# Kernel optimization log

Measured on AMD Instinct MI355X. Metric: run time of the kernel, lower is better.

The kernel has to match this reference:

```python
import jax, jax.numpy as jnp
import numpy as np

N, SEQ_LEN, HORIZON, F_IN, EMBED, HIDDEN, LAYERS = 4096, 168, 24, 32, 32, 64, 2
G4 = 4 * HIDDEN
# NOTE: original torch code calls nn.LSTM per-step WITHOUT carrying hidden state,
# so each step's LSTM starts from (h0=0, c0=0): W_hh contributes nothing, only b_hh.

def setup_inputs() -> dict:
    key = jax.random.key(0)
    ks = jax.random.split(key, 12)
    s = 0.1
    return {
        "X": jax.random.normal(ks[0], (N, SEQ_LEN, F_IN), jnp.float32),
        "y": jax.random.normal(ks[1], (N, SEQ_LEN), jnp.float32),
        "Xf": jax.random.normal(ks[2], (N, HORIZON, F_IN), jnp.float32),
        "W_embed": jax.random.normal(ks[3], (EMBED, 1), jnp.float32) * s,
        "b_embed": jax.random.normal(ks[4], (EMBED,), jnp.float32) * s,
        "W_ih": jax.random.normal(ks[5], (LAYERS, G4, EMBED + F_IN), jnp.float32) * s,  # layer1 in-dim == HIDDEN == EMBED+F_IN
        "b_ih": jax.random.normal(ks[6], (LAYERS, G4), jnp.float32) * s,
        "b_hh": jax.random.normal(ks[7], (LAYERS, G4), jnp.float32) * s,
        "W_mu": jax.random.normal(ks[8], (1, HIDDEN), jnp.float32) * s,
        "b_mu": jax.random.normal(ks[9], (1,), jnp.float32) * s,
        "W_sigma": jax.random.normal(ks[10], (1, HIDDEN), jnp.float32) * s,
        "b_sigma": jax.random.normal(ks[11], (1,), jnp.float32) * s,
    }


def reference(X, y, Xf, W_embed, b_embed, W_ih, b_ih, b_hh, W_mu, b_mu, W_sigma, b_sigma):
    num_ts = X.shape[0]
    T = SEQ_LEN + HORIZON
    Xall = jnp.concatenate([X, Xf], axis=1)  # (N, T, F_IN)
    y_pad = jnp.concatenate([y, jnp.zeros((num_ts, HORIZON), y.dtype)], axis=1)  # (N, T)
    use_y = jnp.arange(T) < SEQ_LEN  # teacher-forced region

    def step(carry, inputs):
        x_s, y_s, use = inputs  # (N, F_IN), (N,), scalar bool
        ynext = jnp.where(use, y_s[:, None], carry)  # (N, 1)
        yembed = ynext @ W_embed.T + b_embed  # (N, EMBED)
        h = jnp.concatenate([x_s, yembed], axis=1)  # (N, F_IN+EMBED)
        for l in range(LAYERS):  # single LSTM step from zero state per layer
            gates = h @ W_ih[l].T + b_ih[l] + b_hh[l]  # (N, 4H); torch gate order i,f,g,o
            i_g, f_g, g_g, o_g = jnp.split(gates, 4, axis=1)
            c = jax.nn.sigmoid(i_g) * jnp.tanh(g_g)  # f * c0 term vanishes (c0 = 0)
            h = jax.nn.sigmoid(o_g) * jnp.tanh(c)
        h = jax.nn.relu(h)
        mu = h @ W_mu.T + b_mu  # (N, 1)
        sigma = jax.nn.softplus(h @ W_sigma.T + b_sigma) + 1e-6  # log(1+exp(.)) + eps
        lik = (2.0 * np.pi * sigma ** 2) ** (-0.5) * jnp.exp(-((ynext - mu) ** 2) / (2.0 * sigma ** 2))
        return lik, (lik[:, 0], mu[:, 0], sigma[:, 0])

    carry0 = jnp.zeros((num_ts, 1), X.dtype)
    xs = (jnp.swapaxes(Xall, 0, 1), y_pad.T, use_y)
    _, (lik_t, mu_t, sigma_t) = jax.lax.scan(step, carry0, xs)  # each (T, N)
    ypred = lik_t.T[:, SEQ_LEN - 1: SEQ_LEN + HORIZON - 1]  # (N, HORIZON)
    return ypred, mu_t.T, sigma_t.T
```

## Files before the change

kernel.cpp:

```cpp
#include <hip/hip_runtime.h>
#include <math.h>

#define N_TS 4096
#define SEQ  168
#define HOR  24
#define T_ALL 192
#define F_INP 32
#define HID  64
#define NROW 192
#define NB_B (N_TS / 16)
#define L2E  1.44269504089f

typedef _Float16 half8  __attribute__((ext_vector_type(8)));
typedef _Float16 half4  __attribute__((ext_vector_type(4)));
typedef float    floatx4 __attribute__((ext_vector_type(4)));

__device__ __forceinline__ float fexp(float x)  { return __expf(x); }
__device__ __forceinline__ float ex2(float x)   { return __builtin_amdgcn_exp2f(x); }
__device__ __forceinline__ float frcp(float x)  { return __builtin_amdgcn_rcpf(x); }
__device__ __forceinline__ float softplus_(float x) { return (x > 15.0f) ? x : __logf(1.0f + fexp(x)); }

__device__ __forceinline__ float lstm_h(float ip, float gp, float op) {
    const float Ei = ex2(ip);
    const float Eg = ex2(gp);
    const float cc = (1.0f - Eg) * frcp((1.0f + Ei) * (1.0f + Eg));
    const float Ec = ex2(cc * (-2.0f * L2E));
    const float Eo = ex2(op);
    return (1.0f - Ec) * frcp((1.0f + Ec) * (1.0f + Eo));
}

__device__ __forceinline__ half8 cvt8(const float4 a, const float4 b) {
    half8 v;
    v[0]=(_Float16)a.x; v[1]=(_Float16)a.y; v[2]=(_Float16)a.z; v[3]=(_Float16)a.w;
    v[4]=(_Float16)b.x; v[5]=(_Float16)b.y; v[6]=(_Float16)b.z; v[7]=(_Float16)b.w;
    return v;
}

__global__ __launch_bounds__(256) void prep(
    const float* __restrict__ W_ih, const float* __restrict__ b_ih,
    const float* __restrict__ b_hh,
    const float* __restrict__ W_embed, const float* __restrict__ b_embed,
    _Float16* __restrict__ W16f, float* __restrict__ bsum,
    float* __restrict__ wy1, float* __restrict__ b1c)
{
    const int idx = blockIdx.x * 256 + threadIdx.x;
    for (int i = idx; i < 2 * 8 * NROW * 8; i += gridDim.x * 256) {
        const int kp  = i & 7;
        const int row = (i >> 3) % NROW;
        const int kb  = ((i >> 3) / NROW) & 7;
        const int l   = i / (8 * NROW * 8);
        const int sr  = (row < 64) ? row : row + 64;
        const float sc = (row >= 64 && row < 128) ? (-2.0f * L2E) : (-L2E);
        W16f[i] = (_Float16)(W_ih[(l * 256 + sr) * HID + kb * 8 + kp] * sc);
    }
    for (int i = idx; i < 2 * NROW; i += gridDim.x * 256) {
        const int r = i % NROW;
        const int l = i / NROW;
        const int sr = (r < 64) ? r : r + 64;
        const float sc = (r >= 64 && r < 128) ? (-2.0f * L2E) : (-L2E);
        bsum[i] = (b_ih[l * 256 + sr] + b_hh[l * 256 + sr]) * sc;
    }
    if (idx < NROW) {
        const int sr = (idx < 64) ? idx : idx + 64;
        const float sc = (idx >= 64 && idx < 128) ? (-2.0f * L2E) : (-L2E);
        const float* wrow = W_ih + sr * HID + 32;
        float s1 = 0.f, s2 = 0.f;
        #pragma unroll
        for (int k = 0; k < 32; ++k) {
            s1 = fmaf(wrow[k], W_embed[k], s1);
            s2 = fmaf(wrow[k], b_embed[k], s2);
        }
        wy1[idx] = s1 * sc;
        b1c[idx] = (b_ih[sr] + b_hh[sr] + s2) * sc;
    }
}

__global__ __launch_bounds__(256, 5) void fused(
    const float* __restrict__ X,
    const float* __restrict__ y,
    const float* __restrict__ Xf,
    const float* __restrict__ W_embed,
    const float* __restrict__ b_embed,
    const _Float16* __restrict__ W16f,
    const float* __restrict__ bsum,
    const float* __restrict__ wy1,
    const float* __restrict__ b1c,
    const float* __restrict__ W_mu,
    const float* __restrict__ b_mu,
    const float* __restrict__ W_sigma,
    const float* __restrict__ b_sigma,
    float* __restrict__ out)
{
    __shared__ union __align__(16) {
        struct { _Float16 Wl[12288]; _Float16 Hx[4][1024]; } A;
        struct { _Float16 slab[16 * 64]; float partm[16][4]; float parts[16][4];
                 float wyb[NROW]; float b1cb[NROW]; } B;
    } sh;

    const int tid = threadIdx.x;
    float* mu_out = out + (size_t)N_TS * HOR;
    float* sg_out = mu_out + (size_t)N_TS * T_ALL;

    if (blockIdx.x < NB_B) {
        __builtin_amdgcn_s_setprio(1);
        const int w    = tid >> 6;
        const int lane = tid & 63;
        const int quad = lane >> 4;
        const int ln   = lane & 15;
        const int n0   = blockIdx.x * 16;

        if (tid < NROW) {
            sh.B.wyb[tid]  = wy1[tid];
            sh.B.b1cb[tid] = b1c[tid];
        }

        half8 B1[3];
        half8 B2[3][2];
        float bias2[3];
        #pragma unroll
        for (int j = 0; j < 3; ++j) {
            const int rt = j * 4 + w;
            B1[j] = *(const half8*)(W16f + ((size_t)quad * NROW + rt * 16 + ln) * 8);
            #pragma unroll
            for (int kt = 0; kt < 2; ++kt)
                B2[j][kt] = *(const half8*)(W16f + 12288 + ((size_t)(kt * 4 + quad) * NROW + rt * 16 + ln) * 8);
            bias2[j] = bsum[NROW + rt * 16 + ln];
        }
        const float wmu = W_mu[w * 16 + ln], wsg = W_sigma[w * 16 + ln];
        const float bmu = b_mu[0], bsg = b_sigma[0];

        const float* xfp = Xf + (size_t)(n0 + ln) * HOR * F_INP + quad * 8;
        float4 xa, xb;
        {
            const float* xp = X + ((size_t)(n0 + ln) * SEQ + (SEQ - 1)) * F_INP + quad * 8;
            xa = *(const float4*)xp;
            xb = *(const float4*)(xp + 4);
        }
        float ycur = y[(size_t)(n0 + ln) * SEQ + (SEQ - 1)];
        __syncthreads();

        #pragma unroll 1
        for (int it = 0; it <= HOR + 1; ++it) {
            if (it > 0) {
                const int k = it - 1;
                const float4 m4 = *(const float4*)sh.B.partm[ln];
                const float4 s4 = *(const float4*)sh.B.parts[ln];
                const float mu = (m4.x + m4.y) + (m4.z + m4.w) + bmu;
                const float sg = softplus_((s4.x + s4.y) + (s4.z + s4.w) + bsg) + 1e-6f;
                const float d  = ycur - mu;
                const float is = frcp(sg);
                const float lik = 0.39894228040143267f * is * fexp(-0.5f * d * d * is * is);
                if (k > 0 && w == 0 && quad == 0) {
                    const int nn = n0 + ln;
                    const int t  = SEQ + k - 1;
                    mu_out[(size_t)nn * T_ALL + t] = mu;
                    sg_out[(size_t)nn * T_ALL + t] = sg;
                    if (k < HOR) out[(size_t)nn * HOR + k] = lik;
                }
                ycur = lik;
            }
            if (it > HOR) break;

            const half8 xf0 = cvt8(xa, xb);
            if (it < HOR) {
                xa = *(const float4*)(xfp + it * F_INP);
                xb = *(const float4*)(xfp + it * F_INP + 4);
            }

            floatx4 t0 = *(const floatx4*)(sh.B.b1cb + 0 * 64 + w * 16 + quad * 4);
            floatx4 t1 = *(const floatx4*)(sh.B.b1cb + 1 * 64 + w * 16 + quad * 4);
            floatx4 t2 = *(const floatx4*)(sh.B.b1cb + 2 * 64 + w * 16 + quad * 4);
            t0 = __builtin_amdgcn_mfma_f32_16x16x32_f16(B1[0], xf0, t0, 0, 0, 0);
            t1 = __builtin_amdgcn_mfma_f32_16x16x32_f16(B1[1], xf0, t1, 0, 0, 0);
            t2 = __builtin_amdgcn_mfma_f32_16x16x32_f16(B1[2], xf0, t2, 0, 0, 0);

            const floatx4 wy0 = *(const floatx4*)(sh.B.wyb + 0 * 64 + w * 16 + quad * 4);
            const floatx4 wy1v = *(const floatx4*)(sh.B.wyb + 1 * 64 + w * 16 + quad * 4);
            const floatx4 wy2 = *(const floatx4*)(sh.B.wyb + 2 * 64 + w * 16 + quad * 4);

            half4 h1p;
            #pragma unroll
            for (int r = 0; r < 4; ++r) {
                const float ig = fmaf(ycur, wy0[r], t0[r]);
                const float gg = fmaf(ycur, wy1v[r], t1[r]);
                const float og = fmaf(ycur, wy2[r], t2[r]);
                h1p[r] = (_Float16)lstm_h(ig, gg, og);
            }
            {
                const int xblk = (2 * w + (quad >> 1)) ^ (ln & 7);
                *(half4*)(&sh.B.slab[ln * 64 + xblk * 8 + (quad & 1) * 4]) = h1p;
            }
            __syncthreads();

            const half8 a0 = *(const half8*)(&sh.B.slab[ln * 64 + ((quad ^ (ln & 7)) << 3)]);
            const half8 a1 = *(const half8*)(&sh.B.slab[ln * 64 + (((4 + quad) ^ (ln & 7)) << 3)]);
            floatx4 acc[3];
            #pragma unroll
            for (int j = 0; j < 3; ++j) {
                acc[j] = (floatx4){bias2[j], bias2[j], bias2[j], bias2[j]};
                acc[j] = __builtin_amdgcn_mfma_f32_16x16x32_f16(a0, B2[j][0], acc[j], 0, 0, 0);
                acc[j] = __builtin_amdgcn_mfma_f32_16x16x32_f16(a1, B2[j][1], acc[j], 0, 0, 0);
            }

            float pmr[4], psr[4];
            #pragma unroll
            for (int r = 0; r < 4; ++r) {
                const float hh = lstm_h(acc[0][r], acc[1][r], acc[2][r]);
                const float hr = fmaxf(hh, 0.0f);
                pmr[r] = hr * wmu;
                psr[r] = hr * wsg;
            }
            #pragma unroll
            for (int off = 1; off < 16; off <<= 1) {
                #pragma unroll
                for (int r = 0; r < 4; ++r) {
                    pmr[r] += __shfl_xor(pmr[r], off, 64);
                    psr[r] += __shfl_xor(psr[r], off, 64);
                }
            }
            if (ln == 0) {
                #pragma unroll
                for (int r = 0; r < 4; ++r) {
                    sh.B.partm[quad * 4 + r][w] = pmr[r];
                    sh.B.parts[quad * 4 + r][w] = psr[r];
                }
            }
            __syncthreads();
        }
        return;
    }

    const int w    = tid >> 6;
    const int lane = tid & 63;
    const int quad = lane >> 4;
    const int ln   = lane & 15;
    const int cid0 = (blockIdx.x - NB_B) * 64 + w * 16;
    const int cid  = cid0 + ln;

    half8 afr0, afr1;
    {
        const float* xp = X + (size_t)cid * F_INP + quad * 8;
        const float4 xa = *(const float4*)xp;
        const float4 xb = *(const float4*)(xp + 4);
        afr0 = cvt8(xa, xb);
        const float yv = y[cid];
        const float4 wa = *(const float4*)(W_embed + quad * 8);
        const float4 wb = *(const float4*)(W_embed + quad * 8 + 4);
        const float4 ba = *(const float4*)(b_embed + quad * 8);
        const float4 bb = *(const float4*)(b_embed + quad * 8 + 4);
        afr1[0]=(_Float16)fmaf(yv, wa.x, ba.x); afr1[1]=(_Float16)fmaf(yv, wa.y, ba.y);
        afr1[2]=(_Float16)fmaf(yv, wa.z, ba.z); afr1[3]=(_Float16)fmaf(yv, wa.w, ba.w);
        afr1[4]=(_Float16)fmaf(yv, wb.x, bb.x); afr1[5]=(_Float16)fmaf(yv, wb.y, bb.y);
        afr1[6]=(_Float16)fmaf(yv, wb.z, bb.z); afr1[7]=(_Float16)fmaf(yv, wb.w, bb.w);
    }

    #pragma unroll
    for (int c = 0; c < 6; ++c) {
        const int off = (c * 256 + tid) * 8;
        *(half8*)(sh.A.Wl + off) = *(const half8*)(W16f + off);
    }
    __syncthreads();

    _Float16* hrow = sh.A.Hx[w];
    {
        const _Float16* bp = sh.A.Wl + quad * 1536 + ln * 8;
        #pragma unroll
        for (int jt = 0; jt < 4; ++jt) {
            const float bi = bsum[jt * 16 + ln];
            const float bg = bsum[(4 + jt) * 16 + ln];
            const float bo = bsum[(8 + jt) * 16 + ln];
            floatx4 ai = (floatx4){bi, bi, bi, bi};
            floatx4 ag = (floatx4){bg, bg, bg, bg};
            floatx4 ao = (floatx4){bo, bo, bo, bo};
            ai = __builtin_amdgcn_mfma_f32_16x16x32_f16(afr0, *(const half8*)(bp + jt * 128),              ai, 0, 0, 0);
            ai = __builtin_amdgcn_mfma_f32_16x16x32_f16(afr1, *(const half8*)(bp + jt * 128 + 6144),       ai, 0, 0, 0);
            ag = __builtin_amdgcn_mfma_f32_16x16x32_f16(afr0, *(const half8*)(bp + (4 + jt) * 128),        ag, 0, 0, 0);
            ag = __builtin_amdgcn_mfma_f32_16x16x32_f16(afr1, *(const half8*)(bp + (4 + jt) * 128 + 6144), ag, 0, 0, 0);
            ao = __builtin_amdgcn_mfma_f32_16x16x32_f16(afr0, *(const half8*)(bp + (8 + jt) * 128),        ao, 0, 0, 0);
            ao = __builtin_amdgcn_mfma_f32_16x16x32_f16(afr1, *(const half8*)(bp + (8 + jt) * 128 + 6144), ao, 0, 0, 0);
            #pragma unroll
            for (int r = 0; r < 4; ++r) {
                const float hh = lstm_h(ai[r], ag[r], ao[r]);
                const int row = quad * 4 + r;
                const int col = jt * 16 + ln;
                hrow[row * 64 + (((col >> 3) ^ (row & 7)) << 3) + (col & 7)] = (_Float16)hh;
            }
        }
    }

    const half8 a0 = *(const half8*)(hrow + ln * 64 + ((quad ^ (ln & 7)) << 3));
    const half8 a1 = *(const half8*)(hrow + ln * 64 + (((4 + quad) ^ (ln & 7)) << 3));

    __syncthreads();
    #pragma unroll
    for (int c = 0; c < 6; ++c) {
        const int off = (c * 256 + tid) * 8;
        *(half8*)(sh.A.Wl + off) = *(const half8*)(W16f + 12288 + off);
    }
    __syncthreads();

    float hfin[4][4];
    {
        const _Float16* bp = sh.A.Wl + quad * 1536 + ln * 8;
        #pragma unroll
        for (int jt = 0; jt < 4; ++jt) {
            const float bi = bsum[NROW + jt * 16 + ln];
            const float bg = bsum[NROW + (4 + jt) * 16 + ln];
            const float bo = bsum[NROW + (8 + jt) * 16 + ln];
            floatx4 ai = (floatx4){bi, bi, bi, bi};
            floatx4 ag = (floatx4){bg, bg, bg, bg};
            floatx4 ao = (floatx4){bo, bo, bo, bo};
            ai = __builtin_amdgcn_mfma_f32_16x16x32_f16(a0, *(const half8*)(bp + jt * 128),              ai, 0, 0, 0);
            ai = __builtin_amdgcn_mfma_f32_16x16x32_f16(a1, *(const half8*)(bp + jt * 128 + 6144),       ai, 0, 0, 0);
            ag = __builtin_amdgcn_mfma_f32_16x16x32_f16(a0, *(const half8*)(bp + (4 + jt) * 128),        ag, 0, 0, 0);
            ag = __builtin_amdgcn_mfma_f32_16x16x32_f16(a1, *(const half8*)(bp + (4 + jt) * 128 + 6144), ag, 0, 0, 0);
            ao = __builtin_amdgcn_mfma_f32_16x16x32_f16(a0, *(const half8*)(bp + (8 + jt) * 128),        ao, 0, 0, 0);
            ao = __builtin_amdgcn_mfma_f32_16x16x32_f16(a1, *(const half8*)(bp + (8 + jt) * 128 + 6144), ao, 0, 0, 0);
            #pragma unroll
            for (int r = 0; r < 4; ++r)
                hfin[jt][r] = lstm_h(ai[r], ag[r], ao[r]);
        }
    }

    float wmu[4], wsg[4];
    #pragma unroll
    for (int jt = 0; jt < 4; ++jt) {
        wmu[jt] = W_mu[jt * 16 + ln];
        wsg[jt] = W_sigma[jt * 16 + ln];
    }
    const float bmu = b_mu[0], bsg = b_sigma[0];

    #pragma unroll
    for (int r = 0; r < 4; ++r) {
        float pm = 0.f, ps = 0.f;
        #pragma unroll
        for (int jt = 0; jt < 4; ++jt) {
            const float hr = fmaxf(hfin[jt][r], 0.0f);
            pm = fmaf(hr, wmu[jt], pm);
            ps = fmaf(hr, wsg[jt], ps);
        }
        #pragma unroll
        for (int off = 1; off < 16; off <<= 1) {
            pm += __shfl_xor(pm, off, 64);
            ps += __shfl_xor(ps, off, 64);
        }
        if (ln == 0) {
            const int cid2 = cid0 + quad * 4 + r;
            const int n = cid2 / SEQ;
            const int t = cid2 - n * SEQ;
            const float mu = pm + bmu;
            const float sg = softplus_(ps + bsg) + 1e-6f;
            mu_out[(size_t)n * T_ALL + t] = mu;
            sg_out[(size_t)n * T_ALL + t] = sg;
            if (t == SEQ - 1) {
                const float yv = y[cid2];
                const float d  = yv - mu;
                const float is = frcp(sg);
                const float lik = 0.39894228040143267f * is * fexp(-0.5f * d * d * is * is);
                out[(size_t)n * HOR] = lik;
            }
        }
    }
}

extern "C" void kernel_launch(void* const* d_in, const int* in_sizes, int n_in,
                              void* d_out, int out_size, void* d_ws, size_t ws_size,
                              hipStream_t stream) {
    const float* X       = (const float*)d_in[0];
    const float* y       = (const float*)d_in[1];
    const float* Xf      = (const float*)d_in[2];
    const float* W_embed = (const float*)d_in[3];
    const float* b_embed = (const float*)d_in[4];
    const float* W_ih    = (const float*)d_in[5];
    const float* b_ih    = (const float*)d_in[6];
    const float* b_hh    = (const float*)d_in[7];
    const float* W_mu    = (const float*)d_in[8];
    const float* b_mu    = (const float*)d_in[9];
    const float* W_sigma = (const float*)d_in[10];
    const float* b_sigma = (const float*)d_in[11];

    float* out = (float*)d_out;
    _Float16*  W16f = (_Float16*)d_ws;
    float*     bsum = (float*)((char*)d_ws + 49152);
    float*     wy1  = (float*)((char*)d_ws + 49152 + 1536);
    float*     b1c  = (float*)((char*)d_ws + 49152 + 1536 + 768);

    prep<<<96, 256, 0, stream>>>(W_ih, b_ih, b_hh, W_embed, b_embed,
                                 W16f, bsum, wy1, b1c);

    fused<<<NB_B + (N_TS * SEQ) / 64, 256, 0, stream>>>(
        X, y, Xf, W_embed, b_embed, W16f, bsum, wy1, b1c,
        W_mu, b_mu, W_sigma, b_sigma, out);
}
```

Before: 249.1 us.

## Fold y-embedding into layer-1 bias, halve layer-1 K, and use 512-thread blocks

The teacher-forced blocks now treat the y-embedding half of layer 1 as a rank-1 term (y*wy1 + b1c) instead of a second K=32 MFMA. This halves layer-1 MFMA work and shrinks the packed layer-1 weights. Blocks grow to 512 threads: autoregressive blocks handle two 16-series groups with separate shared-memory slabs, and teacher-forced blocks cover 128 rows. The mu/sigma head is restructured to use an operand-swapped MFMA layout with a shorter cross-lane reduction, and half-width stores of h. Larger blocks may cut occupancy flexibility and increase the cost of each barrier.

```diff
diff --git a/kernel.cpp b/kernel.cpp
--- a/kernel.cpp
+++ b/kernel.cpp
@@ -8,8 +8,10 @@
 #define F_INP 32
 #define HID  64
 #define NROW 192
-#define NB_B (N_TS / 16)
+#define NB_B (N_TS / 32)
+#define NT_B ((N_TS * SEQ) / 128)
 #define L2E  1.44269504089f
+#define W16F_L1 6144
 
 typedef _Float16 half8  __attribute__((ext_vector_type(8)));
 typedef _Float16 half4  __attribute__((ext_vector_type(4)));
@@ -44,14 +46,21 @@
     float* __restrict__ wy1, float* __restrict__ b1c)
 {
     const int idx = blockIdx.x * 256 + threadIdx.x;
-    for (int i = idx; i < 2 * 8 * NROW * 8; i += gridDim.x * 256) {
+    for (int i = idx; i < 4 * NROW * 8; i += gridDim.x * 256) {
         const int kp  = i & 7;
         const int row = (i >> 3) % NROW;
-        const int kb  = ((i >> 3) / NROW) & 7;
-        const int l   = i / (8 * NROW * 8);
+        const int kb  = (i >> 3) / NROW;
         const int sr  = (row < 64) ? row : row + 64;
         const float sc = (row >= 64 && row < 128) ? (-2.0f * L2E) : (-L2E);
-        W16f[i] = (_Float16)(W_ih[(l * 256 + sr) * HID + kb * 8 + kp] * sc);
+        W16f[i] = (_Float16)(W_ih[sr * HID + kb * 8 + kp] * sc);
+    }
+    for (int i = idx; i < 8 * NROW * 8; i += gridDim.x * 256) {
+        const int kp  = i & 7;
+        const int row = (i >> 3) % NROW;
+        const int kb  = (i >> 3) / NROW;
+        const int sr  = (row < 64) ? row : row + 64;
+        const float sc = (row >= 64 && row < 128) ? (-2.0f * L2E) : (-L2E);
+        W16f[W16F_L1 + i] = (_Float16)(W_ih[(256 + sr) * HID + kb * 8 + kp] * sc);
     }
     for (int i = idx; i < 2 * NROW; i += gridDim.x * 256) {
         const int r = i % NROW;
@@ -75,7 +84,7 @@
     }
 }
 
-__global__ __launch_bounds__(256, 5) void fused(
+__global__ __launch_bounds__(512, 8) void fused(
     const float* __restrict__ X,
     const float* __restrict__ y,
     const float* __restrict__ Xf,
@@ -92,8 +101,8 @@
     float* __restrict__ out)
 {
     __shared__ union __align__(16) {
-        struct { _Float16 Wl[12288]; _Float16 Hx[4][1024]; } A;
-        struct { _Float16 slab[16 * 64]; float partm[16][4]; float parts[16][4];
+        struct { _Float16 Wl[12288]; _Float16 Hx[8][1024]; } A;
+        struct { _Float16 slab[2][1024]; float partm[2][16][4]; float parts[2][16][4];
                  float wyb[NROW]; float b1cb[NROW]; } B;
     } sh;
 
@@ -104,10 +113,12 @@
     if (blockIdx.x < NB_B) {
         __builtin_amdgcn_s_setprio(1);
         const int w    = tid >> 6;
+        const int g    = w >> 2;
+        const int wg   = w & 3;
         const int lane = tid & 63;
         const int quad = lane >> 4;
         const int ln   = lane & 15;
-        const int n0   = blockIdx.x * 16;
+        const int n0   = blockIdx.x * 32 + g * 16;
 
         if (tid < NROW) {
             sh.B.wyb[tid]  = wy1[tid];
@@ -119,14 +130,14 @@
         float bias2[3];
         #pragma unroll
         for (int j = 0; j < 3; ++j) {
-            const int rt = j * 4 + w;
+            const int rt = j * 4 + wg;
             B1[j] = *(const half8*)(W16f + ((size_t)quad * NROW + rt * 16 + ln) * 8);
             #pragma unroll
             for (int kt = 0; kt < 2; ++kt)
-                B2[j][kt] = *(const half8*)(W16f + 12288 + ((size_t)(kt * 4 + quad) * NROW + rt * 16 + ln) * 8);
+                B2[j][kt] = *(const half8*)(W16f + W16F_L1 + ((size_t)(kt * 4 + quad) * NROW + rt * 16 + ln) * 8);
             bias2[j] = bsum[NROW + rt * 16 + ln];
         }
-        const float wmu = W_mu[w * 16 + ln], wsg = W_sigma[w * 16 + ln];
+        const float wmu = W_mu[wg * 16 + ln], wsg = W_sigma[wg * 16 + ln];
         const float bmu = b_mu[0], bsg = b_sigma[0];
 
         const float* xfp = Xf + (size_t)(n0 + ln) * HOR * F_INP + quad * 8;
@@ -143,14 +154,14 @@
         for (int it = 0; it <= HOR + 1; ++it) {
             if (it > 0) {
                 const int k = it - 1;
-                const float4 m4 = *(const float4*)sh.B.partm[ln];
-                const float4 s4 = *(const float4*)sh.B.parts[ln];
+                const float4 m4 = *(const float4*)sh.B.partm[g][ln];
+                const float4 s4 = *(const float4*)sh.B.parts[g][ln];
                 const float mu = (m4.x + m4.y) + (m4.z + m4.w) + bmu;
                 const float sg = softplus_((s4.x + s4.y) + (s4.z + s4.w) + bsg) + 1e-6f;
                 const float d  = ycur - mu;
                 const float is = frcp(sg);
                 const float lik = 0.39894228040143267f * is * fexp(-0.5f * d * d * is * is);
-                if (k > 0 && w == 0 && quad == 0) {
+                if (k > 0 && wg == 0 && quad == 0) {
                     const int nn = n0 + ln;
                     const int t  = SEQ + k - 1;
                     mu_out[(size_t)nn * T_ALL + t] = mu;
@@ -167,33 +178,33 @@
                 xb = *(const float4*)(xfp + it * F_INP + 4);
             }
 
-            floatx4 t0 = *(const floatx4*)(sh.B.b1cb + 0 * 64 + w * 16 + quad * 4);
-            floatx4 t1 = *(const floatx4*)(sh.B.b1cb + 1 * 64 + w * 16 + quad * 4);
-            floatx4 t2 = *(const floatx4*)(sh.B.b1cb + 2 * 64 + w * 16 + quad * 4);
+            floatx4 t0 = *(const floatx4*)(sh.B.b1cb + 0 * 64 + wg * 16 + quad * 4);
+            floatx4 t1 = *(const floatx4*)(sh.B.b1cb + 1 * 64 + wg * 16 + quad * 4);
+            floatx4 t2 = *(const floatx4*)(sh.B.b1cb + 2 * 64 + wg * 16 + quad * 4);
             t0 = __builtin_amdgcn_mfma_f32_16x16x32_f16(B1[0], xf0, t0, 0, 0, 0);
             t1 = __builtin_amdgcn_mfma_f32_16x16x32_f16(B1[1], xf0, t1, 0, 0, 0);
             t2 = __builtin_amdgcn_mfma_f32_16x16x32_f16(B1[2], xf0, t2, 0, 0, 0);
 
-            const floatx4 wy0 = *(const floatx4*)(sh.B.wyb + 0 * 64 + w * 16 + quad * 4);
-            const floatx4 wy1v = *(const floatx4*)(sh.B.wyb + 1 * 64 + w * 16 + quad * 4);
-            const floatx4 wy2 = *(const floatx4*)(sh.B.wyb + 2 * 64 + w * 16 + quad * 4);
+            const floatx4 wy0  = *(const floatx4*)(sh.B.wyb + 0 * 64 + wg * 16 + quad * 4);
+            const floatx4 wy1v = *(const floatx4*)(sh.B.wyb + 1 * 64 + wg * 16 + quad * 4);
+            const floatx4 wy2  = *(const floatx4*)(sh.B.wyb + 2 * 64 + wg * 16 + quad * 4);
 
             half4 h1p;
             #pragma unroll
             for (int r = 0; r < 4; ++r) {
-                const float ig = fmaf(ycur, wy0[r], t0[r]);
+                const float ig = fmaf(ycur, wy0[r],  t0[r]);
                 const float gg = fmaf(ycur, wy1v[r], t1[r]);
-                const float og = fmaf(ycur, wy2[r], t2[r]);
+                const float og = fmaf(ycur, wy2[r],  t2[r]);
                 h1p[r] = (_Float16)lstm_h(ig, gg, og);
             }
             {
-                const int xblk = (2 * w + (quad >> 1)) ^ (ln & 7);
-                *(half4*)(&sh.B.slab[ln * 64 + xblk * 8 + (quad & 1) * 4]) = h1p;
+                const int xblk = (2 * wg + (quad >> 1)) ^ (ln & 7);
+                *(half4*)(&sh.B.slab[g][ln * 64 + xblk * 8 + (quad & 1) * 4]) = h1p;
             }
             __syncthreads();
 
-            const half8 a0 = *(const half8*)(&sh.B.slab[ln * 64 + ((quad ^ (ln & 7)) << 3)]);
-            const half8 a1 = *(const half8*)(&sh.B.slab[ln * 64 + (((4 + quad) ^ (ln & 7)) << 3)]);
+            const half8 a0 = *(const half8*)(&sh.B.slab[g][ln * 64 + ((quad ^ (ln & 7)) << 3)]);
+            const half8 a1 = *(const half8*)(&sh.B.slab[g][ln * 64 + (((4 + quad) ^ (ln & 7)) << 3)]);
             floatx4 acc[3];
             #pragma unroll
             for (int j = 0; j < 3; ++j) {
@@ -221,8 +232,8 @@
             if (ln == 0) {
                 #pragma unroll
                 for (int r = 0; r < 4; ++r) {
-                    sh.B.partm[quad * 4 + r][w] = pmr[r];
-                    sh.B.parts[quad * 4 + r][w] = psr[r];
+                    sh.B.partm[g][quad * 4 + r][wg] = pmr[r];
+                    sh.B.parts[g][quad * 4 + r][wg] = psr[r];
                 }
             }
             __syncthreads();
@@ -234,31 +245,19 @@
     const int lane = tid & 63;
     const int quad = lane >> 4;
     const int ln   = lane & 15;
-    const int cid0 = (blockIdx.x - NB_B) * 64 + w * 16;
+    const int cid0 = (blockIdx.x - NB_B) * 128 + w * 16;
     const int cid  = cid0 + ln;
 
-    half8 afr0, afr1;
+    half8 xfr;
     {
         const float* xp = X + (size_t)cid * F_INP + quad * 8;
-        const float4 xa = *(const float4*)xp;
-        const float4 xb = *(const float4*)(xp + 4);
-        afr0 = cvt8(xa, xb);
-        const float yv = y[cid];
-        const float4 wa = *(const float4*)(W_embed + quad * 8);
-        const float4 wb = *(const float4*)(W_embed + quad * 8 + 4);
-        const float4 ba = *(const float4*)(b_embed + quad * 8);
-        const float4 bb = *(const float4*)(b_embed + quad * 8 + 4);
-        afr1[0]=(_Float16)fmaf(yv, wa.x, ba.x); afr1[1]=(_Float16)fmaf(yv, wa.y, ba.y);
-        afr1[2]=(_Float16)fmaf(yv, wa.z, ba.z); afr1[3]=(_Float16)fmaf(yv, wa.w, ba.w);
-        afr1[4]=(_Float16)fmaf(yv, wb.x, bb.x); afr1[5]=(_Float16)fmaf(yv, wb.y, bb.y);
-        afr1[6]=(_Float16)fmaf(yv, wb.z, bb.z); afr1[7]=(_Float16)fmaf(yv, wb.w, bb.w);
-    }
-
-    #pragma unroll
-    for (int c = 0; c < 6; ++c) {
-        const int off = (c * 256 + tid) * 8;
-        *(half8*)(sh.A.Wl + off) = *(const half8*)(W16f + off);
-    }
+        xfr = cvt8(*(const float4*)xp, *(const float4*)(xp + 4));
+    }
+    const float yv = y[cid];
+
+    *(half8*)(sh.A.Wl + (size_t)tid * 8) = *(const half8*)(W16f + (size_t)tid * 8);
+    if (tid < 256)
+        *(half8*)(sh.A.Wl + (size_t)(512 + tid) * 8) = *(const half8*)(W16f + (size_t)(512 + tid) * 8);
     __syncthreads();
 
     _Float16* hrow = sh.A.Hx[w];
@@ -266,99 +265,73 @@
         const _Float16* bp = sh.A.Wl + quad * 1536 + ln * 8;
         #pragma unroll
         for (int jt = 0; jt < 4; ++jt) {
-            const float bi = bsum[jt * 16 + ln];
-            const float bg = bsum[(4 + jt) * 16 + ln];
-            const float bo = bsum[(8 + jt) * 16 + ln];
-            floatx4 ai = (floatx4){bi, bi, bi, bi};
-            floatx4 ag = (floatx4){bg, bg, bg, bg};
-            floatx4 ao = (floatx4){bo, bo, bo, bo};
-            ai = __builtin_amdgcn_mfma_f32_16x16x32_f16(afr0, *(const half8*)(bp + jt * 128),              ai, 0, 0, 0);
-            ai = __builtin_amdgcn_mfma_f32_16x16x32_f16(afr1, *(const half8*)(bp + jt * 128 + 6144),       ai, 0, 0, 0);
-            ag = __builtin_amdgcn_mfma_f32_16x16x32_f16(afr0, *(const half8*)(bp + (4 + jt) * 128),        ag, 0, 0, 0);
-            ag = __builtin_amdgcn_mfma_f32_16x16x32_f16(afr1, *(const half8*)(bp + (4 + jt) * 128 + 6144), ag, 0, 0, 0);
-            ao = __builtin_amdgcn_mfma_f32_16x16x32_f16(afr0, *(const half8*)(bp + (8 + jt) * 128),        ao, 0, 0, 0);
-            ao = __builtin_amdgcn_mfma_f32_16x16x32_f16(afr1, *(const half8*)(bp + (8 + jt) * 128 + 6144), ao, 0, 0, 0);
+            floatx4 ai = *(const floatx4*)(b1c + jt * 16 + quad * 4);
+            floatx4 ag = *(const floatx4*)(b1c + 64 + jt * 16 + quad * 4);
+            floatx4 ao = *(const floatx4*)(b1c + 128 + jt * 16 + quad * 4);
+            ai = __builtin_amdgcn_mfma_f32_16x16x32_f16(*(const half8*)(bp + jt * 128),        xfr, ai, 0, 0, 0);
+            ag = __builtin_amdgcn_mfma_f32_16x16x32_f16(*(const half8*)(bp + 512 + jt * 128),  xfr, ag, 0, 0, 0);
+            ao = __builtin_amdgcn_mfma_f32_16x16x32_f16(*(const half8*)(bp + 1024 + jt * 128), xfr, ao, 0, 0, 0);
+            const floatx4 wyi = *(const floatx4*)(wy1 + jt * 16 + quad * 4);
+            const floatx4 wyg = *(const floatx4*)(wy1 + 64 + jt * 16 + quad * 4);
+            const floatx4 wyo = *(const floatx4*)(wy1 + 128 + jt * 16 + quad * 4);
+            half4 h1p;
             #pragma unroll
             for (int r = 0; r < 4; ++r) {
-                const float hh = lstm_h(ai[r], ag[r], ao[r]);
-                const int row = quad * 4 + r;
-                const int col = jt * 16 + ln;
-                hrow[row * 64 + (((col >> 3) ^ (row & 7)) << 3) + (col & 7)] = (_Float16)hh;
-            }
-        }
-    }
-
+                h1p[r] = (_Float16)lstm_h(fmaf(yv, wyi[r], ai[r]),
+                                          fmaf(yv, wyg[r], ag[r]),
+                                          fmaf(yv, wyo[r], ao[r]));
+            }
+            const int xblk = (jt * 2 + (quad >> 1)) ^ (ln & 7);
+            *(half4*)(&hrow[ln * 64 + xblk * 8 + (quad & 1) * 4]) = h1p;
+        }
+    }
     const half8 a0 = *(const half8*)(hrow + ln * 64 + ((quad ^ (ln & 7)) << 3));
     const half8 a1 = *(const half8*)(hrow + ln * 64 + (((4 + quad) ^ (ln & 7)) << 3));
 
     __syncthreads();
-    #pragma unroll
-    for (int c = 0; c < 6; ++c) {
-        const int off = (c * 256 + tid) * 8;
-        *(half8*)(sh.A.Wl + off) = *(const half8*)(W16f + 12288 + off);
-    }
+    *(half8*)(sh.A.Wl + (size_t)tid * 8)          = *(const half8*)(W16f + W16F_L1 + (size_t)tid * 8);
+    *(half8*)(sh.A.Wl + (size_t)(512 + tid) * 8)  = *(const half8*)(W16f + W16F_L1 + (size_t)(512 + tid) * 8);
+    *(half8*)(sh.A.Wl + (size_t)(1024 + tid) * 8) = *(const half8*)(W16f + W16F_L1 + (size_t)(1024 + tid) * 8);
     __syncthreads();
 
-    float hfin[4][4];
+    float pm = 0.f, ps = 0.f;
     {
         const _Float16* bp = sh.A.Wl + quad * 1536 + ln * 8;
         #pragma unroll
         for (int jt = 0; jt < 4; ++jt) {
-            const float bi = bsum[NROW + jt * 16 + ln];
-            const float bg = bsum[NROW + (4 + jt) * 16 + ln];
-            const float bo = bsum[NROW + (8 + jt) * 16 + ln];
-            floatx4 ai = (floatx4){bi, bi, bi, bi};
-            floatx4 ag = (floatx4){bg, bg, bg, bg};
-            floatx4 ao = (floatx4){bo, bo, bo, bo};
-            ai = __builtin_amdgcn_mfma_f32_16x16x32_f16(a0, *(const half8*)(bp + jt * 128),              ai, 0, 0, 0);
-            ai = __builtin_amdgcn_mfma_f32_16x16x32_f16(a1, *(const half8*)(bp + jt * 128 + 6144),       ai, 0, 0, 0);
-            ag = __builtin_amdgcn_mfma_f32_16x16x32_f16(a0, *(const half8*)(bp + (4 + jt) * 128),        ag, 0, 0, 0);
-            ag = __builtin_amdgcn_mfma_f32_16x16x32_f16(a1, *(const half8*)(bp + (4 + jt) * 128 + 6144), ag, 0, 0, 0);
-            ao = __builtin_amdgcn_mfma_f32_16x16x32_f16(a0, *(const half8*)(bp + (8 + jt) * 128),        ao, 0, 0, 0);
-            ao = __builtin_amdgcn_mfma_f32_16x16x32_f16(a1, *(const half8*)(bp + (8 + jt) * 128 + 6144), ao, 0, 0, 0);
-            #pragma unroll
-            for (int r = 0; r < 4; ++r)
-                hfin[jt][r] = lstm_h(ai[r], ag[r], ao[r]);
-        }
-    }
-
-    float wmu[4], wsg[4];
-    #pragma unroll
-    for (int jt = 0; jt < 4; ++jt) {
-        wmu[jt] = W_mu[jt * 16 + ln];
-        wsg[jt] = W_sigma[jt * 16 + ln];
-    }
-    const float bmu = b_mu[0], bsg = b_sigma[0];
-
-    #pragma unroll
-    for (int r = 0; r < 4; ++r) {
-        float pm = 0.f, ps = 0.f;
-        #pragma unroll
-        for (int jt = 0; jt < 4; ++jt) {
-            const float hr = fmaxf(hfin[jt][r], 0.0f);
-            pm = fmaf(hr, wmu[jt], pm);
-            ps = fmaf(hr, wsg[jt], ps);
-        }
-        #pragma unroll
-        for (int off = 1; off < 16; off <<= 1) {
-            pm += __shfl_xor(pm, off, 64);
-            ps += __shfl_xor(ps, off, 64);
-        }
-        if (ln == 0) {
-            const int cid2 = cid0 + quad * 4 + r;
-            const int n = cid2 / SEQ;
-            const int t = cid2 - n * SEQ;
-            const float mu = pm + bmu;
-            const float sg = softplus_(ps + bsg) + 1e-6f;
-            mu_out[(size_t)n * T_ALL + t] = mu;
-            sg_out[(size_t)n * T_ALL + t] = sg;
-            if (t == SEQ - 1) {
-                const float yv = y[cid2];
-                const float d  = yv - mu;
-                const float is = frcp(sg);
-                const float lik = 0.39894228040143267f * is * fexp(-0.5f * d * d * is * is);
-                out[(size_t)n * HOR] = lik;
-            }
+            floatx4 ai = *(const floatx4*)(bsum + NROW + jt * 16 + quad * 4);
+            floatx4 ag = *(const floatx4*)(bsum + NROW + 64 + jt * 16 + quad * 4);
+            floatx4 ao = *(const floatx4*)(bsum + NROW + 128 + jt * 16 + quad * 4);
+            ai = __builtin_amdgcn_mfma_f32_16x16x32_f16(*(const half8*)(bp + jt * 128),               a0, ai, 0, 0, 0);
+            ai = __builtin_amdgcn_mfma_f32_16x16x32_f16(*(const half8*)(bp + 6144 + jt * 128),        a1, ai, 0, 0, 0);
+            ag = __builtin_amdgcn_mfma_f32_16x16x32_f16(*(const half8*)(bp + 512 + jt * 128),         a0, ag, 0, 0, 0);
+            ag = __builtin_amdgcn_mfma_f32_16x16x32_f16(*(const half8*)(bp + 6144 + 512 + jt * 128),  a1, ag, 0, 0, 0);
+            ao = __builtin_amdgcn_mfma_f32_16x16x32_f16(*(const half8*)(bp + 1024 + jt * 128),        a0, ao, 0, 0, 0);
+            ao = __builtin_amdgcn_mfma_f32_16x16x32_f16(*(const half8*)(bp + 6144 + 1024 + jt * 128), a1, ao, 0, 0, 0);
+            const floatx4 wm  = *(const floatx4*)(W_mu + jt * 16 + quad * 4);
+            const floatx4 ws4 = *(const floatx4*)(W_sigma + jt * 16 + quad * 4);
+            #pragma unroll
+            for (int r = 0; r < 4; ++r) {
+                const float hr = fmaxf(lstm_h(ai[r], ag[r], ao[r]), 0.0f);
+                pm = fmaf(hr, wm[r], pm);
+                ps = fmaf(hr, ws4[r], ps);
+            }
+        }
+    }
+    pm += __shfl_xor(pm, 16, 64); pm += __shfl_xor(pm, 32, 64);
+    ps += __shfl_xor(ps, 16, 64); ps += __shfl_xor(ps, 32, 64);
+
+    if (quad == 0) {
+        const int n = cid / SEQ;
+        const int t = cid - n * SEQ;
+        const float mu = pm + b_mu[0];
+        const float sg = softplus_(ps + b_sigma[0]) + 1e-6f;
+        mu_out[(size_t)n * T_ALL + t] = mu;
+        sg_out[(size_t)n * T_ALL + t] = sg;
+        if (t == SEQ - 1) {
+            const float d  = yv - mu;
+            const float is = frcp(sg);
+            out[(size_t)n * HOR] = 0.39894228040143267f * is * fexp(-0.5f * d * d * is * is);
         }
     }
 }
@@ -381,14 +354,14 @@
 
     float* out = (float*)d_out;
     _Float16*  W16f = (_Float16*)d_ws;
-    float*     bsum = (float*)((char*)d_ws + 49152);
-    float*     wy1  = (float*)((char*)d_ws + 49152 + 1536);
-    float*     b1c  = (float*)((char*)d_ws + 49152 + 1536 + 768);
+    float*     bsum = (float*)((char*)d_ws + 36864);
+    float*     wy1  = (float*)((char*)d_ws + 36864 + 1536);
+    float*     b1c  = (float*)((char*)d_ws + 36864 + 1536 + 768);
 
     prep<<<96, 256, 0, stream>>>(W_ih, b_ih, b_hh, W_embed, b_embed,
                                  W16f, bsum, wy1, b1c);
 
-    fused<<<NB_B + (N_TS * SEQ) / 64, 256, 0, stream>>>(
+    fused<<<NB_B + NT_B, 512, 0, stream>>>(
         X, y, Xf, W_embed, b_embed, W16f, bsum, wy1, b1c,
         W_mu, b_mu, W_sigma, b_sigma, out);
 }
```

Result: slower. 276.0 us (+10.8%).
